# Performance work log

Hardware: AMD Instinct MI355X
Metric: run time of the kernel (lower is better)

## Reference

```python
import jax, jax.numpy as jnp
import numpy as np

N = 100000   # nodes
E = 200000   # edges
D = 512      # in_features
H = 512      # out_features


def setup_inputs() -> dict:
    key = jax.random.key(0)
    ks = jax.random.split(key, 12)
    s = 0.04  # ~1/sqrt(512), keeps gates out of saturation like nn.Linear init
    rng = np.random.default_rng(0)
    edge_index = jnp.asarray(rng.integers(0, N, size=(2, E)), dtype=jnp.int32)
    return {
        "x": jax.random.normal(ks[0], (N, D), jnp.float32),
        "edge_index": edge_index,
        "edge_feats": jax.random.normal(ks[1], (10, D), jnp.float32),
        "edge_types": jax.random.uniform(ks[2], (E, 10), jnp.float32),
        "W_iou_w": jax.random.normal(ks[3], (3 * H, D), jnp.float32) * s,
        "W_iou_b": jax.random.normal(ks[4], (3 * H,), jnp.float32) * s,
        "U_iou_w": jax.random.normal(ks[5], (3 * H, H), jnp.float32) * s,
        "U_iou_b": jax.random.normal(ks[6], (3 * H,), jnp.float32) * s,
        "W_f_w": jax.random.normal(ks[7], (H, D), jnp.float32) * s,
        "W_f_b": jax.random.normal(ks[8], (H,), jnp.float32) * s,
        "U_f_w": jax.random.normal(ks[9], (H, H), jnp.float32) * s,
        "U_f_b": jax.random.normal(ks[10], (H,), jnp.float32) * s,
    }


def _orders(parents, n_nodes):
    """node_order[p] = #edges with parent p; edge_order[i] = 1-based rank of edge i
    among same-parent edges in edge-list order (matches the torch python loop)."""
    e = parents.shape[0]
    node_order = np.zeros(n_nodes, dtype=np.int64)
    np.add.at(node_order, parents, 1)
    order = np.argsort(parents, kind="stable")
    sp = parents[order]
    is_new = np.ones(e, dtype=bool)
    is_new[1:] = sp[1:] != sp[:-1]
    pos = np.arange(e)
    start = pos[is_new][np.cumsum(is_new) - 1]  # start index of each parent group
    edge_order = np.zeros(e, dtype=np.int64)
    edge_order[order] = pos - start + 1
    return node_order, edge_order


def reference(x, edge_index, edge_feats, edge_types, W_iou_w, W_iou_b,
              U_iou_w, U_iou_b, W_f_w, W_f_b, U_f_w, U_f_b):
    # edge_feats / edge_types are unused in the default (untyped) path, as in the torch code.
    ei = np.asarray(edge_index)
    parents, children = ei[0], ei[1]
    n_nodes = x.shape[0]
    out_f = W_f_b.shape[0]
    node_order, edge_order = _orders(parents, n_nodes)
    max_iter = int(node_order.max()) if parents.size else 0

    h = jnp.zeros((n_nodes, out_f), x.dtype)
    c = jnp.zeros((n_nodes, out_f), x.dtype)
    h_sum = jnp.zeros((n_nodes, out_f), x.dtype)

    for n in range(max_iter + 1):
        nm = np.nonzero(node_order == n)[0]       # nodes evaluated this wavefront
        xn = x[nm]
        if n == 0:
            iou = xn @ W_iou_w.T + W_iou_b
        else:
            em = np.nonzero(edge_order == n)[0]   # n-th child edge of each parent
            p, ch = parents[em], children[em]     # p is unique within a wavefront
            child_h = h[ch]
            child_c = c[ch]
            h_sum = h_sum.at[p].add(child_h)
            iou = xn @ W_iou_w.T + W_iou_b + h_sum[nm] @ U_iou_w.T + U_iou_b
        i, o, u = jnp.split(iou, 3, axis=1)
        i, o, u = jax.nn.sigmoid(i), jax.nn.sigmoid(o), jnp.tanh(u)
        c = c.at[nm].set(i * u)
        if n > 0:
            f = jax.nn.sigmoid(x[p] @ W_f_w.T + W_f_b + child_h @ U_f_w.T + U_f_b)
            c = c.at[p].add(f * child_c)
        h = h.at[nm].set(o * jnp.tanh(c[nm]))
    return h
```

## Files before the change

### kernel.cpp

```cpp
#include <hip/hip_runtime.h>
#include <math.h>

#define MAXIT 16
#define MAXDEG 16

typedef __attribute__((ext_vector_type(8))) short bf16x8;
typedef __attribute__((ext_vector_type(16))) float f32x16;

static inline int imin(int a, int b) { return a < b ? a : b; }

__device__ __forceinline__ float sigm(float v) { return 1.0f / (1.0f + __expf(-v)); }
__device__ __forceinline__ float tfast(float v) {
  float vc = fminf(fmaxf(v, -20.0f), 20.0f);
  float t = __expf(2.0f * vc);
  return (t - 1.0f) / (t + 1.0f);
}
__device__ __forceinline__ unsigned short f2bf(float f) {
  unsigned int u = __float_as_uint(f);
  u += 0x7FFFu + ((u >> 16) & 1u);
  return (unsigned short)(u >> 16);
}
__device__ __forceinline__ float bf2f(unsigned short s) {
  return __uint_as_float(((unsigned int)s) << 16);
}
__device__ __forceinline__ unsigned bfadd2(unsigned x, unsigned y) {
  float sl = bf2f((unsigned short)(x & 0xFFFFu)) + bf2f((unsigned short)(y & 0xFFFFu));
  float sh = bf2f((unsigned short)(x >> 16)) + bf2f((unsigned short)(y >> 16));
  return (unsigned)f2bf(sl) | ((unsigned)f2bf(sh) << 16);
}
__device__ __forceinline__ uint4 bfadd8(uint4 a, uint4 b) {
  return make_uint4(bfadd2(a.x, b.x), bfadd2(a.y, b.y), bfadd2(a.z, b.z), bfadd2(a.w, b.w));
}

__global__ void kzero16(uint4* p, size_t n) {
  size_t i = (size_t)blockIdx.x * blockDim.x + threadIdx.x;
  size_t st = (size_t)gridDim.x * blockDim.x;
  uint4 z = make_uint4(0u, 0u, 0u, 0u);
  for (; i < n; i += st) p[i] = z;
}
__global__ void kzeroi(int* p, int n) {
  int i = blockIdx.x * blockDim.x + threadIdx.x;
  if (i < n) p[i] = 0;
}
__global__ void kfill(float* p, size_t n, float v) {
  size_t i = (size_t)blockIdx.x * blockDim.x + threadIdx.x;
  size_t st = (size_t)gridDim.x * blockDim.x;
  for (; i < n; i += st) p[i] = v;
}

__global__ void k_histo(const int* __restrict__ par, int E,
                        int* __restrict__ node_order, int* __restrict__ bucket) {
  int e = blockIdx.x * blockDim.x + threadIdx.x;
  if (e >= E) return;
  int p = par[e];
  int slot = atomicAdd(&node_order[p], 1);
  if (slot < MAXDEG) bucket[(size_t)p * MAXDEG + slot] = e;
}

__global__ void k_rank(const int* __restrict__ par, int E, int N,
                       const int* __restrict__ node_order, const int* __restrict__ bucket,
                       int* __restrict__ edgeCnt, int* __restrict__ edgeList) {
  __shared__ int lcnt[MAXIT], lbase[MAXIT];
  const int t = threadIdx.x;
  if (t < MAXIT) lcnt[t] = 0;
  __syncthreads();
  int e = blockIdx.x * blockDim.x + t;
  int r = 0, ls = 0;
  if (e < E) {
    int p = par[e];
    int d = node_order[p]; if (d > MAXDEG) d = MAXDEG;
    int rr = 1;
    for (int j = 0; j < d; ++j) rr += (bucket[(size_t)p * MAXDEG + j] < e) ? 1 : 0;
    if (rr < MAXIT) { r = rr; ls = atomicAdd(&lcnt[rr], 1); }
  }
  __syncthreads();
  if (t < MAXIT && lcnt[t] > 0) lbase[t] = atomicAdd(&edgeCnt[t], lcnt[t]);
  __syncthreads();
  if (r > 0) edgeList[(size_t)r * N + lbase[r] + ls] = e;
}

__global__ void k_nodelist(int N, const int* __restrict__ node_order,
                           int* __restrict__ nodeCnt, int* __restrict__ nodeList) {
  __shared__ int lcnt[MAXIT], lbase[MAXIT];
  const int t = threadIdx.x;
  if (t < MAXIT) lcnt[t] = 0;
  __syncthreads();
  int v = blockIdx.x * blockDim.x + t;
  int n = -1, ls = 0;
  if (v < N) {
    n = node_order[v]; if (n >= MAXIT) n = MAXIT - 1;
    ls = atomicAdd(&lcnt[n], 1);
  }
  __syncthreads();
  if (t < MAXIT && lcnt[t] > 0) lbase[t] = atomicAdd(&nodeCnt[t], lcnt[t]);
  __syncthreads();
  if (n >= 0) nodeList[(size_t)n * N + lbase[n] + ls] = v;
}

__global__ void k_pack_x(const float* __restrict__ x, unsigned short* __restrict__ xb, size_t n8) {
  size_t i = (size_t)blockIdx.x * blockDim.x + threadIdx.x;
  size_t st = (size_t)gridDim.x * blockDim.x;
  for (; i < n8; i += st) {
    const float* p = x + i * 8;
    float4 f0 = *(const float4*)p, f1 = *(const float4*)(p + 4);
    uint4 r;
    r.x = (unsigned)f2bf(f0.x) | ((unsigned)f2bf(f0.y) << 16);
    r.y = (unsigned)f2bf(f0.z) | ((unsigned)f2bf(f0.w) << 16);
    r.z = (unsigned)f2bf(f1.x) | ((unsigned)f2bf(f1.y) << 16);
    r.w = (unsigned)f2bf(f1.z) | ((unsigned)f2bf(f1.w) << 16);
    *(uint4*)(xb + i * 8) = r;
  }
}

__global__ void k_pack_biou(const float* __restrict__ W, const float* __restrict__ U,
                            unsigned short* __restrict__ Bpk) {
  int i = blockIdx.x * blockDim.x + threadIdx.x;
  if (i >= 16 * 64 * 3 * 64) return;
  int lane = i & 63;
  int q = i >> 6;
  int g = q % 3; q /= 3;
  int s = q & 63;
  int jc = q >> 6;
  int col = jc * 32 + (lane & 31);
  int k0 = s * 16 + (lane >> 5) * 8;
  int rowW = g * 512 + col;
  unsigned short v[8];
#pragma unroll
  for (int j = 0; j < 8; ++j) {
    int kk = k0 + j;
    v[j] = f2bf(kk < 512 ? W[(size_t)rowW * 512 + kk] : U[(size_t)rowW * 512 + kk - 512]);
  }
  *(uint4*)(Bpk + (size_t)i * 8) = *(uint4*)v;
}

__global__ void k_pack_bf(const float* __restrict__ W, const float* __restrict__ U,
                          unsigned short* __restrict__ Bpk) {
  int i = blockIdx.x * blockDim.x + threadIdx.x;
  if (i >= 16 * 64 * 64) return;
  int lane = i & 63;
  int q = i >> 6;
  int s = q & 63;
  int jc = q >> 6;
  int col = jc * 32 + (lane & 31);
  int k0 = s * 16 + (lane >> 5) * 8;
  unsigned short v[8];
#pragma unroll
  for (int j = 0; j < 8; ++j) {
    int kk = k0 + j;
    v[j] = f2bf(kk < 512 ? W[(size_t)col * 512 + kk] : U[(size_t)col * 512 + kk - 512]);
  }
  *(uint4*)(Bpk + (size_t)i * 8) = *(uint4*)v;
}

__global__ void k_edge_pre(int n, int N, const int* __restrict__ edgeCnt, const int* __restrict__ edgeList,
                           const int* __restrict__ par, const int* __restrict__ chd,
                           const int* __restrict__ node_order,
                           const unsigned short* __restrict__ hb, unsigned short* __restrict__ hsumb,
                           const unsigned short* __restrict__ fc, float* __restrict__ c) {
  const int cntH = edgeCnt[n];
  const int cntA = (n >= 2) ? edgeCnt[n - 1] : 0;
  const size_t totH = (size_t)cntH * 64;
  const size_t total = totH + (size_t)cntA * 64;
  size_t st = (size_t)gridDim.x * blockDim.x;
  for (size_t i = (size_t)blockIdx.x * blockDim.x + threadIdx.x; i < total; i += st) {
    if (i < totH) {
      int slot = (int)(i >> 6), j8 = ((int)i & 63) << 3;
      int e = edgeList[(size_t)n * N + slot];
      int p = par[e], ch = chd[e];
      uint4 hv = *(const uint4*)&hb[(size_t)ch * 512 + j8];
      if (n == 1) {
        *(uint4*)&hsumb[(size_t)p * 512 + j8] = hv;
      } else {
        uint4 hs = *(const uint4*)&hsumb[(size_t)p * 512 + j8];
        *(uint4*)&hsumb[(size_t)p * 512 + j8] = bfadd8(hs, hv);
      }
    } else {
      size_t k = i - totH;
      int slot = (int)(k >> 6), j8 = ((int)k & 63) << 3;
      int e = edgeList[(size_t)(n - 1) * N + slot];
      int p = par[e];
      if (node_order[p] <= n - 1) continue;
      size_t base = (size_t)p * 512 + j8;
      uint4 f8 = *(const uint4*)&fc[base];
      unsigned fw[4] = {f8.x, f8.y, f8.z, f8.w};
      float4 c0 = *(const float4*)&c[base];
      float4 c1 = *(const float4*)&c[base + 4];
      c0.x += bf2f((unsigned short)(fw[0] & 0xFFFFu)); c0.y += bf2f((unsigned short)(fw[0] >> 16));
      c0.z += bf2f((unsigned short)(fw[1] & 0xFFFFu)); c0.w += bf2f((unsigned short)(fw[1] >> 16));
      c1.x += bf2f((unsigned short)(fw[2] & 0xFFFFu)); c1.y += bf2f((unsigned short)(fw[2] >> 16));
      c1.z += bf2f((unsigned short)(fw[3] & 0xFFFFu)); c1.w += bf2f((unsigned short)(fw[3] >> 16));
      *(float4*)&c[base] = c0;
      *(float4*)&c[base + 4] = c1;
    }
  }
}

template<int MODE>
__global__ __launch_bounds__(256, 2)
void k_gemm9(int n, int N, const int* __restrict__ cntArr, const int* __restrict__ list,
             const int* __restrict__ par, const int* __restrict__ chd,
             const unsigned short* __restrict__ xb, const unsigned short* __restrict__ hsrc,
             const unsigned short* __restrict__ Bpk,
             const float* __restrict__ bW, const float* __restrict__ bU,
             float* __restrict__ c, float* __restrict__ h, unsigned short* __restrict__ hb,
             unsigned short* __restrict__ fc) {
  const int cnt = cntArr[n];
  if (cnt == 0) return;
  constexpr int KS    = (MODE == 0) ? 32 : 64;
  constexpr int KC8   = KS * 2;
  constexpr int GATES = (MODE == 2) ? 1 : 3;
  constexpr int NSTR  = (MODE == 2) ? 2 : 1;
  constexpr int NPASS = (MODE == 2) ? 2 : 4;
  constexpr int D     = 4;
  const int rowTiles = (cnt + 31) >> 5;

  __shared__ uint4 lA4[KS * 64];
  __shared__ int ids0[32], ids1[32];
  const int t = threadIdx.x, lane = t & 63, w = t >> 6;

  auto ldA = [&](int s) -> bf16x8 {
    int hk = lane >> 5, rl = lane & 31;
    return *(const bf16x8*)&lA4[s * 64 + hk * 32 + (rl ^ ((2 * s + hk) & 31))];
  };

  for (int tile = blockIdx.x; tile < rowTiles; tile += gridDim.x) {
    __syncthreads();
    if (t < 32) {
      int r = (tile << 5) + t;
      int idx = (r < cnt) ? list[(size_t)n * N + r] : -1;
      if (MODE == 2) { ids0[t] = idx >= 0 ? par[idx] : -1; ids1[t] = idx >= 0 ? chd[idx] : 0; }
      else           { ids0[t] = idx; ids1[t] = 0; }
    }
    __syncthreads();

    constexpr int ITERS = (32 * KC8) / 256;
#pragma unroll
    for (int i = 0; i < ITERS; ++i) {
      int cid = i * 256 + t;
      int row = cid >> ((MODE == 0) ? 6 : 7);
      int kc8 = cid & (KC8 - 1);
      int id0 = ids0[row];
      int id = id0 < 0 ? 0 : id0;
      uint4 v;
      if (MODE == 0 || kc8 < 64) {
        v = *(const uint4*)(xb + (size_t)id * 512 + (kc8 << 3));
      } else {
        int idh = (MODE == 2) ? ids1[row] : id;
        v = *(const uint4*)(hsrc + (size_t)idh * 512 + ((kc8 - 64) << 3));
      }
      int s = kc8 >> 1, hk = kc8 & 1;
      lA4[s * 64 + hk * 32 + (row ^ (kc8 & 31))] = v;
    }
    __syncthreads();

    for (int p = 0; p < NPASS; ++p) {
      const uint4* bb[NSTR];
#pragma unroll
      for (int str = 0; str < NSTR; ++str) {
        int jc = (MODE == 2) ? (p * 8 + str * 4 + w) : (p * 4 + w);
        bb[str] = (const uint4*)Bpk + (size_t)jc * 64 * GATES * 64 + lane;
      }
      f32x16 acc[NSTR][GATES];
#pragma unroll
      for (int str = 0; str < NSTR; ++str)
#pragma unroll
        for (int g = 0; g < GATES; ++g)
#pragma unroll
          for (int q = 0; q < 16; ++q) acc[str][g][q] = 0.f;

      bf16x8 aP[D];
      uint4 bP[D][NSTR * GATES];
#pragma unroll
      for (int d = 0; d < D; ++d) {
        aP[d] = ldA(d);
#pragma unroll
        for (int str = 0; str < NSTR; ++str)
#pragma unroll
          for (int g = 0; g < GATES; ++g)
            bP[d][str * GATES + g] = bb[str][(size_t)(d * GATES + g) * 64];
      }
      for (int s0 = 0; s0 < KS - D; s0 += D) {
#pragma unroll
        for (int d = 0; d < D; ++d) {
#pragma unroll
          for (int str = 0; str < NSTR; ++str)
#pragma unroll
            for (int g = 0; g < GATES; ++g)
              acc[str][g] = __builtin_amdgcn_mfma_f32_32x32x16_bf16(
                  aP[d], *(bf16x8*)&bP[d][str * GATES + g], acc[str][g], 0, 0, 0);
          aP[d] = ldA(s0 + D + d);
#pragma unroll
          for (int str = 0; str < NSTR; ++str)
#pragma unroll
            for (int g = 0; g < GATES; ++g)
              bP[d][str * GATES + g] = bb[str][(size_t)((s0 + D + d) * GATES + g) * 64];
        }
      }
#pragma unroll
      for (int d = 0; d < D; ++d)
#pragma unroll
        for (int str = 0; str < NSTR; ++str)
#pragma unroll
          for (int g = 0; g < GATES; ++g)
            acc[str][g] = __builtin_amdgcn_mfma_f32_32x32x16_bf16(
                aP[d], *(bf16x8*)&bP[d][str * GATES + g], acc[str][g], 0, 0, 0);

#pragma unroll
      for (int str = 0; str < NSTR; ++str) {
        const int jc = (MODE == 2) ? (p * 8 + str * 4 + w) : (p * 4 + w);
        const int jh = jc * 32 + (lane & 31);
        if (MODE < 2) {
          float bi = bW[jh], bo = bW[512 + jh], bu = bW[1024 + jh];
          if (MODE == 1) { bi += bU[jh]; bo += bU[512 + jh]; bu += bU[1024 + jh]; }
#pragma unroll
          for (int reg = 0; reg < 16; ++reg) {
            int rl = ((lane >> 5) << 2) + (reg & 3) + ((reg >> 2) << 3);
            int node = ids0[rl];
            if (node < 0) continue;
            size_t base = (size_t)node * 512 + jh;
            float iv = acc[str][0][reg] + bi;
            float ov = acc[str][1][reg] + bo;
            float uv = acc[str][2][reg] + bu;
            float fcv = (MODE == 1) ? bf2f(fc[base]) : 0.f;
            float cn = sigm(iv) * tfast(uv) + fcv;
            c[base] = cn;
            float hv = sigm(ov) * tfast(cn);
            h[base] = hv;
            hb[base] = f2bf(hv);
          }
        } else {
          float bfv = bW[jh] + bU[jh];
#pragma unroll
          for (int reg = 0; reg < 16; ++reg) {
            int rl = ((lane >> 5) << 2) + (reg & 3) + ((reg >> 2) << 3);
            int pe = ids0[rl];
            if (pe < 0) continue;
            int ce = ids1[rl];
            float fv = sigm(acc[str][0][reg] + bfv);
            fc[(size_t)pe * 512 + jh] = f2bf(fv * c[(size_t)ce * 512 + jh]);
          }
        }
      }
    }
  }
}

static void run_all(const float* x, const int* par, const int* chd,
                    const float* Wiou, const float* bWiou, const float* Uiou, const float* bUiou,
                    const float* Wf, const float* bWf, const float* Uf, const float* bUf,
                    float* h, int N, int E, void* d_ws, hipStream_t stream) {
  const size_t NV = (size_t)N * 512;
  char* cur = (char*)d_ws;
  auto take = [&](size_t bytes) -> char* {
    char* r = cur; cur += (bytes + 255) & ~(size_t)255; return r;
  };
  float* c             = (float*)take(NV * 4);
  unsigned short* hb   = (unsigned short*)take(NV * 2);
  unsigned short* hsumb= (unsigned short*)take(NV * 2);
  unsigned short* xb   = (unsigned short*)take(NV * 2);
  unsigned short* fc   = (unsigned short*)take(NV * 2);
  unsigned short* BpkI = (unsigned short*)take((size_t)16 * 64 * 3 * 64 * 8 * 2);
  unsigned short* BpkF = (unsigned short*)take((size_t)16 * 64 * 64 * 8 * 2);
  int* node_order      = (int*)take((size_t)N * 4);
  int* nodeCnt         = (int*)take(MAXIT * 4);
  int* edgeCnt         = (int*)take(MAXIT * 4);
  int* bucket          = (int*)take((size_t)N * MAXDEG * 4);
  int* nodeList        = (int*)take((size_t)MAXIT * N * 4);
  int* edgeList        = (int*)take((size_t)MAXIT * N * 4);

  kzero16<<<2048, 256, 0, stream>>>((uint4*)c, NV * 4 / 16);
  kzero16<<<2048, 256, 0, stream>>>((uint4*)hb, NV * 2 / 16);
  kzeroi<<<(N + 255) / 256, 256, 0, stream>>>(node_order, N);
  kzeroi<<<1, 64, 0, stream>>>(nodeCnt, MAXIT);
  kzeroi<<<1, 64, 0, stream>>>(edgeCnt, MAXIT);

  k_pack_x<<<2048, 256, 0, stream>>>(x, xb, NV / 8);
  k_pack_biou<<<(16 * 64 * 3 * 64 + 255) / 256, 256, 0, stream>>>(Wiou, Uiou, BpkI);
  k_pack_bf<<<(16 * 64 * 64 + 255) / 256, 256, 0, stream>>>(Wf, Uf, BpkF);

  k_histo<<<(E + 255) / 256, 256, 0, stream>>>(par, E, node_order, bucket);
  k_rank<<<(E + 255) / 256, 256, 0, stream>>>(par, E, N, node_order, bucket, edgeCnt, edgeList);
  k_nodelist<<<(N + 255) / 256, 256, 0, stream>>>(N, node_order, nodeCnt, nodeList);

  {
    int g = imin(4096, (N + 31) >> 5);
    k_gemm9<0><<<g, 256, 0, stream>>>(0, N, nodeCnt, nodeList, par, chd,
                                      xb, hsumb, BpkI, bWiou, bUiou, c, h, hb, fc);
  }
  for (int n = 1; n < MAXIT; ++n) {
    int boundE = E / n;
    int boundN = imin(N, boundE);
    int boundA = (n >= 2) ? (E / (n - 1)) : 0;
    int gE = imin(2048, (int)(((size_t)(boundE + boundA) * 64 + 255) / 256));
    int gF = imin(4096, (boundE + 31) >> 5);
    int gI = imin(4096, (boundN + 31) >> 5);
    k_edge_pre<<<gE, 256, 0, stream>>>(n, N, edgeCnt, edgeList, par, chd, node_order,
                                       hb, hsumb, fc, c);
    k_gemm9<2><<<gF, 256, 0, stream>>>(n, N, edgeCnt, edgeList, par, chd,
                                       xb, hb, BpkF, bWf, bUf, c, h, hb, fc);
    k_gemm9<1><<<gI, 256, 0, stream>>>(n, N, nodeCnt, nodeList, par, chd,
                                       xb, hsumb, BpkI, bWiou, bUiou, c, h, hb, fc);
  }
}

extern "C" void kernel_launch(void* const* d_in, const int* in_sizes, int n_in,
                              void* d_out, int out_size, void* d_ws, size_t ws_size,
                              hipStream_t stream) {
  (void)n_in; (void)out_size;
  const float* x     = (const float*)d_in[0];
  const int*   ei    = (const int*)d_in[1];
  const float* Wiou  = (const float*)d_in[4];
  const float* bWiou = (const float*)d_in[5];
  const float* Uiou  = (const float*)d_in[6];
  const float* bUiou = (const float*)d_in[7];
  const float* Wf    = (const float*)d_in[8];
  const float* bWf   = (const float*)d_in[9];
  const float* Uf    = (const float*)d_in[10];
  const float* bUf   = (const float*)d_in[11];
  const int N = in_sizes[0] / 512;
  const int E = in_sizes[1] / 2;
  const int* par = ei;
  const int* chd = ei + E;
  float* h = (float*)d_out;

  const size_t NV = (size_t)N * 512;
  const size_t need = NV * 4 + NV * 2 * 4 +
                      (size_t)8 * 1024 * 1024 +
                      ((size_t)N * (1 + MAXDEG + 2 * MAXIT) + 256) * 4;

  if (ws_size >= need) {
    run_all(x, par, chd, Wiou, bWiou, Uiou, bUiou, Wf, bWf, Uf, bUf,
            h, N, E, d_ws, stream);
  } else {
    kfill<<<2048, 256, 0, stream>>>(h, NV, 1.0e6f);
  }
}
```

Before: 2.626 ms.

## Split forget-gate GEMM into dedicated kernel with single-pass K-halved staging

Moves the forget-gate (MODE 2) path out of the shared templated GEMM into a dedicated kernel. Each wave now computes four 32-column strips in one pass instead of two passes of two strips, so the gathered A tile is read from LDS once per strip group rather than repeatedly. The A tile is staged in two K-halves (x rows, then child h rows) through a half-size LDS buffer. This should cut LDS footprint and reloads, at the cost of more accumulator registers per thread and an extra barrier between halves.

```diff
diff --git a/kernel.cpp b/kernel.cpp
--- a/kernel.cpp
+++ b/kernel.cpp
@@ -208,14 +208,12 @@
   if (cnt == 0) return;
   constexpr int KS    = (MODE == 0) ? 32 : 64;
   constexpr int KC8   = KS * 2;
-  constexpr int GATES = (MODE == 2) ? 1 : 3;
-  constexpr int NSTR  = (MODE == 2) ? 2 : 1;
-  constexpr int NPASS = (MODE == 2) ? 2 : 4;
+  constexpr int GATES = 3;
   constexpr int D     = 4;
   const int rowTiles = (cnt + 31) >> 5;
 
   __shared__ uint4 lA4[KS * 64];
-  __shared__ int ids0[32], ids1[32];
+  __shared__ int ids0[32];
   const int t = threadIdx.x, lane = t & 63, w = t >> 6;
 
   auto ldA = [&](int s) -> bf16x8 {
@@ -227,9 +225,7 @@
     __syncthreads();
     if (t < 32) {
       int r = (tile << 5) + t;
-      int idx = (r < cnt) ? list[(size_t)n * N + r] : -1;
-      if (MODE == 2) { ids0[t] = idx >= 0 ? par[idx] : -1; ids1[t] = idx >= 0 ? chd[idx] : 0; }
-      else           { ids0[t] = idx; ids1[t] = 0; }
+      ids0[t] = (r < cnt) ? list[(size_t)n * N + r] : -1;
     }
     __syncthreads();
 
@@ -245,101 +241,177 @@
       if (MODE == 0 || kc8 < 64) {
         v = *(const uint4*)(xb + (size_t)id * 512 + (kc8 << 3));
       } else {
-        int idh = (MODE == 2) ? ids1[row] : id;
-        v = *(const uint4*)(hsrc + (size_t)idh * 512 + ((kc8 - 64) << 3));
+        v = *(const uint4*)(hsrc + (size_t)id * 512 + ((kc8 - 64) << 3));
       }
       int s = kc8 >> 1, hk = kc8 & 1;
       lA4[s * 64 + hk * 32 + (row ^ (kc8 & 31))] = v;
     }
     __syncthreads();
 
-    for (int p = 0; p < NPASS; ++p) {
-      const uint4* bb[NSTR];
-#pragma unroll
-      for (int str = 0; str < NSTR; ++str) {
-        int jc = (MODE == 2) ? (p * 8 + str * 4 + w) : (p * 4 + w);
-        bb[str] = (const uint4*)Bpk + (size_t)jc * 64 * GATES * 64 + lane;
-      }
-      f32x16 acc[NSTR][GATES];
-#pragma unroll
-      for (int str = 0; str < NSTR; ++str)
-#pragma unroll
-        for (int g = 0; g < GATES; ++g)
-#pragma unroll
-          for (int q = 0; q < 16; ++q) acc[str][g][q] = 0.f;
+    for (int p = 0; p < 4; ++p) {
+      const int jc = p * 4 + w;
+      const uint4* bb = (const uint4*)Bpk + (size_t)jc * 64 * GATES * 64 + lane;
+
+      f32x16 acc[GATES];
+#pragma unroll
+      for (int g = 0; g < GATES; ++g)
+#pragma unroll
+        for (int q = 0; q < 16; ++q) acc[g][q] = 0.f;
 
       bf16x8 aP[D];
-      uint4 bP[D][NSTR * GATES];
+      uint4 bP[D][GATES];
 #pragma unroll
       for (int d = 0; d < D; ++d) {
         aP[d] = ldA(d);
 #pragma unroll
-        for (int str = 0; str < NSTR; ++str)
+        for (int g = 0; g < GATES; ++g)
+          bP[d][g] = bb[(size_t)(d * GATES + g) * 64];
+      }
+      for (int s0 = 0; s0 < KS - D; s0 += D) {
+#pragma unroll
+        for (int d = 0; d < D; ++d) {
 #pragma unroll
           for (int g = 0; g < GATES; ++g)
-            bP[d][str * GATES + g] = bb[str][(size_t)(d * GATES + g) * 64];
-      }
-      for (int s0 = 0; s0 < KS - D; s0 += D) {
-#pragma unroll
-        for (int d = 0; d < D; ++d) {
-#pragma unroll
-          for (int str = 0; str < NSTR; ++str)
-#pragma unroll
-            for (int g = 0; g < GATES; ++g)
-              acc[str][g] = __builtin_amdgcn_mfma_f32_32x32x16_bf16(
-                  aP[d], *(bf16x8*)&bP[d][str * GATES + g], acc[str][g], 0, 0, 0);
+            acc[g] = __builtin_amdgcn_mfma_f32_32x32x16_bf16(
+                aP[d], *(bf16x8*)&bP[d][g], acc[g], 0, 0, 0);
           aP[d] = ldA(s0 + D + d);
 #pragma unroll
-          for (int str = 0; str < NSTR; ++str)
-#pragma unroll
-            for (int g = 0; g < GATES; ++g)
-              bP[d][str * GATES + g] = bb[str][(size_t)((s0 + D + d) * GATES + g) * 64];
+          for (int g = 0; g < GATES; ++g)
+            bP[d][g] = bb[(size_t)((s0 + D + d) * GATES + g) * 64];
         }
       }
 #pragma unroll
       for (int d = 0; d < D; ++d)
 #pragma unroll
-        for (int str = 0; str < NSTR; ++str)
-#pragma unroll
-          for (int g = 0; g < GATES; ++g)
-            acc[str][g] = __builtin_amdgcn_mfma_f32_32x32x16_bf16(
-                aP[d], *(bf16x8*)&bP[d][str * GATES + g], acc[str][g], 0, 0, 0);
-
-#pragma unroll
-      for (int str = 0; str < NSTR; ++str) {
-        const int jc = (MODE == 2) ? (p * 8 + str * 4 + w) : (p * 4 + w);
-        const int jh = jc * 32 + (lane & 31);
-        if (MODE < 2) {
-          float bi = bW[jh], bo = bW[512 + jh], bu = bW[1024 + jh];
-          if (MODE == 1) { bi += bU[jh]; bo += bU[512 + jh]; bu += bU[1024 + jh]; }
-#pragma unroll
-          for (int reg = 0; reg < 16; ++reg) {
-            int rl = ((lane >> 5) << 2) + (reg & 3) + ((reg >> 2) << 3);
-            int node = ids0[rl];
-            if (node < 0) continue;
-            size_t base = (size_t)node * 512 + jh;
-            float iv = acc[str][0][reg] + bi;
-            float ov = acc[str][1][reg] + bo;
-            float uv = acc[str][2][reg] + bu;
-            float fcv = (MODE == 1) ? bf2f(fc[base]) : 0.f;
-            float cn = sigm(iv) * tfast(uv) + fcv;
-            c[base] = cn;
-            float hv = sigm(ov) * tfast(cn);
-            h[base] = hv;
-            hb[base] = f2bf(hv);
-          }
-        } else {
-          float bfv = bW[jh] + bU[jh];
-#pragma unroll
-          for (int reg = 0; reg < 16; ++reg) {
-            int rl = ((lane >> 5) << 2) + (reg & 3) + ((reg >> 2) << 3);
-            int pe = ids0[rl];
-            if (pe < 0) continue;
-            int ce = ids1[rl];
-            float fv = sigm(acc[str][0][reg] + bfv);
-            fc[(size_t)pe * 512 + jh] = f2bf(fv * c[(size_t)ce * 512 + jh]);
-          }
-        }
+        for (int g = 0; g < GATES; ++g)
+          acc[g] = __builtin_amdgcn_mfma_f32_32x32x16_bf16(
+              aP[d], *(bf16x8*)&bP[d][g], acc[g], 0, 0, 0);
+
+      const int jh = jc * 32 + (lane & 31);
+      float bi = bW[jh], bo = bW[512 + jh], bu = bW[1024 + jh];
+      if (MODE == 1) { bi += bU[jh]; bo += bU[512 + jh]; bu += bU[1024 + jh]; }
+#pragma unroll
+      for (int reg = 0; reg < 16; ++reg) {
+        int rl = ((lane >> 5) << 2) + (reg & 3) + ((reg >> 2) << 3);
+        int node = ids0[rl];
+        if (node < 0) continue;
+        size_t base = (size_t)node * 512 + jh;
+        float iv = acc[0][reg] + bi;
+        float ov = acc[1][reg] + bo;
+        float uv = acc[2][reg] + bu;
+        float fcv = (MODE == 1) ? bf2f(fc[base]) : 0.f;
+        float cn = sigm(iv) * tfast(uv) + fcv;
+        c[base] = cn;
+        float hv = sigm(ov) * tfast(cn);
+        h[base] = hv;
+        hb[base] = f2bf(hv);
+      }
+    }
+  }
+}
+
+__global__ __launch_bounds__(256, 2)
+void k_gemmF(int n, int N, const int* __restrict__ edgeCnt, const int* __restrict__ edgeList,
+             const int* __restrict__ par, const int* __restrict__ chd,
+             const unsigned short* __restrict__ xb, const unsigned short* __restrict__ hb,
+             const unsigned short* __restrict__ Bpk,
+             const float* __restrict__ bWf, const float* __restrict__ bUf,
+             const float* __restrict__ c, unsigned short* __restrict__ fc) {
+  const int cnt = edgeCnt[n];
+  if (cnt == 0) return;
+  const int rowTiles = (cnt + 31) >> 5;
+
+  __shared__ uint4 lA4[32 * 64];
+  __shared__ int ids0[32], ids1[32];
+  const int t = threadIdx.x, lane = t & 63, w = t >> 6;
+
+  auto ldA = [&](int s) -> bf16x8 {
+    int hk = lane >> 5, rl = lane & 31;
+    return *(const bf16x8*)&lA4[s * 64 + hk * 32 + (rl ^ ((2 * s + hk) & 31))];
+  };
+
+  for (int tile = blockIdx.x; tile < rowTiles; tile += gridDim.x) {
+    __syncthreads();
+    if (t < 32) {
+      int r = (tile << 5) + t;
+      int idx = (r < cnt) ? edgeList[(size_t)n * N + r] : -1;
+      ids0[t] = idx >= 0 ? par[idx] : -1;
+      ids1[t] = idx >= 0 ? chd[idx] : 0;
+    }
+
+    const uint4* bb[4];
+#pragma unroll
+    for (int str = 0; str < 4; ++str)
+      bb[str] = (const uint4*)Bpk + (size_t)(str * 4 + w) * 64 * 64 + lane;
+
+    f32x16 acc[4];
+#pragma unroll
+    for (int str = 0; str < 4; ++str)
+#pragma unroll
+      for (int q = 0; q < 16; ++q) acc[str][q] = 0.f;
+    __syncthreads();
+
+#pragma unroll
+    for (int half = 0; half < 2; ++half) {
+      if (half) __syncthreads();
+#pragma unroll
+      for (int i = 0; i < 8; ++i) {
+        int cid = i * 256 + t;
+        int row = cid >> 6;
+        int kc8 = cid & 63;
+        int id = half ? ids1[row] : ids0[row];
+        if (id < 0) id = 0;
+        const unsigned short* src = half ? hb : xb;
+        uint4 v = *(const uint4*)(src + (size_t)id * 512 + (kc8 << 3));
+        int s = kc8 >> 1, hk = kc8 & 1;
+        lA4[s * 64 + hk * 32 + (row ^ (kc8 & 31))] = v;
+      }
+      __syncthreads();
+
+      const int sg = half * 32;
+      bf16x8 a0 = ldA(0), a1 = ldA(1);
+      uint4 b0[4], b1[4];
+#pragma unroll
+      for (int str = 0; str < 4; ++str) {
+        b0[str] = bb[str][(size_t)(sg + 0) * 64];
+        b1[str] = bb[str][(size_t)(sg + 1) * 64];
+      }
+      for (int s0 = 0; s0 < 30; s0 += 2) {
+#pragma unroll
+        for (int str = 0; str < 4; ++str)
+          acc[str] = __builtin_amdgcn_mfma_f32_32x32x16_bf16(a0, *(bf16x8*)&b0[str], acc[str], 0, 0, 0);
+        a0 = ldA(s0 + 2);
+#pragma unroll
+        for (int str = 0; str < 4; ++str)
+          b0[str] = bb[str][(size_t)(sg + s0 + 2) * 64];
+#pragma unroll
+        for (int str = 0; str < 4; ++str)
+          acc[str] = __builtin_amdgcn_mfma_f32_32x32x16_bf16(a1, *(bf16x8*)&b1[str], acc[str], 0, 0, 0);
+        a1 = ldA(s0 + 3);
+#pragma unroll
+        for (int str = 0; str < 4; ++str)
+          b1[str] = bb[str][(size_t)(sg + s0 + 3) * 64];
+      }
+#pragma unroll
+      for (int str = 0; str < 4; ++str)
+        acc[str] = __builtin_amdgcn_mfma_f32_32x32x16_bf16(a0, *(bf16x8*)&b0[str], acc[str], 0, 0, 0);
+#pragma unroll
+      for (int str = 0; str < 4; ++str)
+        acc[str] = __builtin_amdgcn_mfma_f32_32x32x16_bf16(a1, *(bf16x8*)&b1[str], acc[str], 0, 0, 0);
+    }
+
+#pragma unroll
+    for (int str = 0; str < 4; ++str) {
+      const int jh = (str * 4 + w) * 32 + (lane & 31);
+      float bfv = bWf[jh] + bUf[jh];
+#pragma unroll
+      for (int reg = 0; reg < 16; ++reg) {
+        int rl = ((lane >> 5) << 2) + (reg & 3) + ((reg >> 2) << 3);
+        int pe = ids0[rl];
+        if (pe < 0) continue;
+        int ce = ids1[rl];
+        float fv = sigm(acc[str][reg] + bfv);
+        fc[(size_t)pe * 512 + jh] = f2bf(fv * c[(size_t)ce * 512 + jh]);
       }
     }
   }
@@ -396,8 +468,8 @@
     int gI = imin(4096, (boundN + 31) >> 5);
     k_edge_pre<<<gE, 256, 0, stream>>>(n, N, edgeCnt, edgeList, par, chd, node_order,
                                        hb, hsumb, fc, c);
-    k_gemm9<2><<<gF, 256, 0, stream>>>(n, N, edgeCnt, edgeList, par, chd,
-                                       xb, hb, BpkF, bWf, bUf, c, h, hb, fc);
+    k_gemmF<<<gF, 256, 0, stream>>>(n, N, edgeCnt, edgeList, par, chd,
+                                    xb, hb, BpkF, bWf, bUf, c, fc);
     k_gemm9<1><<<gI, 256, 0, stream>>>(n, N, nodeCnt, nodeList, par, chd,
                                        xb, hsumb, BpkI, bWiou, bUiou, c, h, hb, fc);
   }
```

Measured after the change: 7.548 ms. 2.87x slower.

## Precompute x·W projections for all nodes in one dense GEMM before wavefronts

Applied to the files above, without the earlier changes.

Adds a dense bf16 MFMA GEMM that computes x·[W_iou;W_f]^T for every node up front into a bf16 buffer, so the per-wavefront gather GEMMs only multiply the hidden-state part (K=512 instead of 1024). Wave 0 becomes a pure elementwise kernel reading the precomputed projections. This removes the repeated x gathers and halves the K loop in the sequential wavefront kernels. In exchange it spends a large up-front GEMM over all N nodes, uses extra workspace of about N*4 KB, and rounds the x projection to bf16. The old path is kept as a fallback when workspace is insufficient.

```diff
diff --git a/kernel.cpp b/kernel.cpp
--- a/kernel.cpp
+++ b/kernel.cpp
@@ -149,6 +149,56 @@
     int kk = k0 + j;
     v[j] = f2bf(kk < 512 ? W[(size_t)col * 512 + kk] : U[(size_t)col * 512 + kk - 512]);
   }
+  *(uint4*)(Bpk + (size_t)i * 8) = *(uint4*)v;
+}
+
+__global__ void k_pack_u3(const float* __restrict__ U, unsigned short* __restrict__ Bpk) {
+  int i = blockIdx.x * blockDim.x + threadIdx.x;
+  if (i >= 16 * 32 * 3 * 64) return;
+  int lane = i & 63;
+  int q = i >> 6;
+  int g = q % 3; q /= 3;
+  int s = q & 31;
+  int jc = q >> 5;
+  int col = jc * 32 + (lane & 31);
+  int k0 = s * 16 + (lane >> 5) * 8;
+  int rowW = g * 512 + col;
+  unsigned short v[8];
+#pragma unroll
+  for (int j = 0; j < 8; ++j) v[j] = f2bf(U[(size_t)rowW * 512 + k0 + j]);
+  *(uint4*)(Bpk + (size_t)i * 8) = *(uint4*)v;
+}
+
+__global__ void k_pack_uf(const float* __restrict__ U, unsigned short* __restrict__ Bpk) {
+  int i = blockIdx.x * blockDim.x + threadIdx.x;
+  if (i >= 16 * 32 * 64) return;
+  int lane = i & 63;
+  int q = i >> 6;
+  int s = q & 31;
+  int jc = q >> 5;
+  int col = jc * 32 + (lane & 31);
+  int k0 = s * 16 + (lane >> 5) * 8;
+  unsigned short v[8];
+#pragma unroll
+  for (int j = 0; j < 8; ++j) v[j] = f2bf(U[(size_t)col * 512 + k0 + j]);
+  *(uint4*)(Bpk + (size_t)i * 8) = *(uint4*)v;
+}
+
+__global__ void k_pack_wx(const float* __restrict__ Wiou, const float* __restrict__ Wf,
+                          unsigned short* __restrict__ Bpk) {
+  int i = blockIdx.x * blockDim.x + threadIdx.x;
+  if (i >= 64 * 32 * 64) return;
+  int lane = i & 63;
+  int q = i >> 6;
+  int s = q & 31;
+  int jc = q >> 5;
+  int col = jc * 32 + (lane & 31);
+  int k0 = s * 16 + (lane >> 5) * 8;
+  const float* src = (col < 1536) ? (Wiou + (size_t)col * 512)
+                                  : (Wf + (size_t)(col - 1536) * 512);
+  unsigned short v[8];
+#pragma unroll
+  for (int j = 0; j < 8; ++j) v[j] = f2bf(src[k0 + j]);
   *(uint4*)(Bpk + (size_t)i * 8) = *(uint4*)v;
 }
 
@@ -345,10 +395,298 @@
   }
 }
 
-static void run_all(const float* x, const int* par, const int* chd,
-                    const float* Wiou, const float* bWiou, const float* Uiou, const float* bUiou,
-                    const float* Wf, const float* bWf, const float* Uf, const float* bUf,
-                    float* h, int N, int E, void* d_ws, hipStream_t stream) {
+__global__ __launch_bounds__(256, 2)
+void k_pxiou(int N, const float* __restrict__ x, const unsigned short* __restrict__ BpkX,
+             unsigned short* __restrict__ px) {
+  const int rowTiles = (N + 31) >> 5;
+  __shared__ uint4 lA4[32 * 64];
+  const int t = threadIdx.x, lane = t & 63, w = t >> 6;
+
+  auto ldA = [&](int s) -> bf16x8 {
+    int hk = lane >> 5, rl = lane & 31;
+    return *(const bf16x8*)&lA4[s * 64 + hk * 32 + (rl ^ ((2 * s + hk) & 31))];
+  };
+
+  for (int tile = blockIdx.x; tile < rowTiles; tile += gridDim.x) {
+    __syncthreads();
+#pragma unroll
+    for (int i = 0; i < 8; ++i) {
+      int cid = i * 256 + t;
+      int row = cid >> 6;
+      int kc8 = cid & 63;
+      int grow = (tile << 5) + row;
+      if (grow >= N) grow = N - 1;
+      const float* p = x + (size_t)grow * 512 + (kc8 << 3);
+      float4 f0 = *(const float4*)p, f1 = *(const float4*)(p + 4);
+      uint4 v;
+      v.x = (unsigned)f2bf(f0.x) | ((unsigned)f2bf(f0.y) << 16);
+      v.y = (unsigned)f2bf(f0.z) | ((unsigned)f2bf(f0.w) << 16);
+      v.z = (unsigned)f2bf(f1.x) | ((unsigned)f2bf(f1.y) << 16);
+      v.w = (unsigned)f2bf(f1.z) | ((unsigned)f2bf(f1.w) << 16);
+      int s = kc8 >> 1, hk = kc8 & 1;
+      lA4[s * 64 + hk * 32 + (row ^ (kc8 & 31))] = v;
+    }
+    __syncthreads();
+
+    for (int p = 0; p < 16; ++p) {
+      const int jc = p * 4 + w;
+      const uint4* bb = (const uint4*)BpkX + (size_t)jc * 32 * 64 + lane;
+      f32x16 acc;
+#pragma unroll
+      for (int q = 0; q < 16; ++q) acc[q] = 0.f;
+      bf16x8 aP[4];
+      uint4 bP[4];
+#pragma unroll
+      for (int d = 0; d < 4; ++d) { aP[d] = ldA(d); bP[d] = bb[(size_t)d * 64]; }
+      for (int s0 = 0; s0 < 28; s0 += 4) {
+#pragma unroll
+        for (int d = 0; d < 4; ++d) {
+          acc = __builtin_amdgcn_mfma_f32_32x32x16_bf16(aP[d], *(bf16x8*)&bP[d], acc, 0, 0, 0);
+          aP[d] = ldA(s0 + 4 + d);
+          bP[d] = bb[(size_t)(s0 + 4 + d) * 64];
+        }
+      }
+#pragma unroll
+      for (int d = 0; d < 4; ++d)
+        acc = __builtin_amdgcn_mfma_f32_32x32x16_bf16(aP[d], *(bf16x8*)&bP[d], acc, 0, 0, 0);
+
+      const int jh = jc * 32 + (lane & 31);
+#pragma unroll
+      for (int reg = 0; reg < 16; ++reg) {
+        int rl = ((lane >> 5) << 2) + (reg & 3) + ((reg >> 2) << 3);
+        int grow = (tile << 5) + rl;
+        if (grow < N) px[(size_t)grow * 2048 + jh] = f2bf(acc[reg]);
+      }
+    }
+  }
+}
+
+__global__ void k_wave0(int N, const int* __restrict__ nodeCnt, const int* __restrict__ nodeList,
+                        const unsigned short* __restrict__ px, const float* __restrict__ bW,
+                        float* __restrict__ c, float* __restrict__ h, unsigned short* __restrict__ hb) {
+  size_t total = (size_t)nodeCnt[0] * 512;
+  size_t st = (size_t)gridDim.x * blockDim.x;
+  for (size_t i = (size_t)blockIdx.x * blockDim.x + threadIdx.x; i < total; i += st) {
+    int slot = (int)(i >> 9), col = (int)(i & 511);
+    int node = nodeList[slot];
+    size_t pb = (size_t)node * 2048;
+    float iv = bf2f(px[pb + col]) + bW[col];
+    float ov = bf2f(px[pb + 512 + col]) + bW[512 + col];
+    float uv = bf2f(px[pb + 1024 + col]) + bW[1024 + col];
+    float cn = sigm(iv) * tfast(uv);
+    size_t base = (size_t)node * 512 + col;
+    c[base] = cn;
+    float hv = sigm(ov) * tfast(cn);
+    h[base] = hv;
+    hb[base] = f2bf(hv);
+  }
+}
+
+template<int MODE>
+__global__ __launch_bounds__(256, 2)
+void k_gemmS(int n, int N, const int* __restrict__ cntArr, const int* __restrict__ list,
+             const int* __restrict__ par, const int* __restrict__ chd,
+             const unsigned short* __restrict__ asrc, const unsigned short* __restrict__ Bpk,
+             const unsigned short* __restrict__ px,
+             const float* __restrict__ bW, const float* __restrict__ bU,
+             float* __restrict__ c, float* __restrict__ h, unsigned short* __restrict__ hb,
+             unsigned short* __restrict__ fc) {
+  const int cnt = cntArr[n];
+  if (cnt == 0) return;
+  constexpr int KS    = 32;
+  constexpr int GATES = (MODE == 2) ? 1 : 3;
+  constexpr int NSTR  = (MODE == 2) ? 2 : 1;
+  constexpr int NPASS = (MODE == 2) ? 2 : 4;
+  constexpr int D     = 4;
+  const int rowTiles = (cnt + 31) >> 5;
+
+  __shared__ uint4 lA4[KS * 64];
+  __shared__ int ids0[32], ids1[32];
+  const int t = threadIdx.x, lane = t & 63, w = t >> 6;
+
+  auto ldA = [&](int s) -> bf16x8 {
+    int hk = lane >> 5, rl = lane & 31;
+    return *(const bf16x8*)&lA4[s * 64 + hk * 32 + (rl ^ ((2 * s + hk) & 31))];
+  };
+
+  for (int tile = blockIdx.x; tile < rowTiles; tile += gridDim.x) {
+    __syncthreads();
+    if (t < 32) {
+      int r = (tile << 5) + t;
+      int idx = (r < cnt) ? list[(size_t)n * N + r] : -1;
+      if (MODE == 2) { ids0[t] = idx >= 0 ? par[idx] : -1; ids1[t] = idx >= 0 ? chd[idx] : 0; }
+      else           { ids0[t] = idx; ids1[t] = 0; }
+    }
+    __syncthreads();
+
+#pragma unroll
+    for (int i = 0; i < 8; ++i) {
+      int cid = i * 256 + t;
+      int row = cid >> 6;
+      int kc8 = cid & 63;
+      int id = (MODE == 2) ? ids1[row] : ids0[row];
+      if (id < 0) id = 0;
+      uint4 v = *(const uint4*)(asrc + (size_t)id * 512 + (kc8 << 3));
+      int s = kc8 >> 1, hk = kc8 & 1;
+      lA4[s * 64 + hk * 32 + (row ^ (kc8 & 31))] = v;
+    }
+    __syncthreads();
+
+    for (int p = 0; p < NPASS; ++p) {
+      const uint4* bb[NSTR];
+#pragma unroll
+      for (int str = 0; str < NSTR; ++str) {
+        int jc = (MODE == 2) ? (p * 8 + str * 4 + w) : (p * 4 + w);
+        bb[str] = (const uint4*)Bpk + (size_t)jc * KS * GATES * 64 + lane;
+      }
+      f32x16 acc[NSTR][GATES];
+#pragma unroll
+      for (int str = 0; str < NSTR; ++str)
+#pragma unroll
+        for (int g = 0; g < GATES; ++g)
+#pragma unroll
+          for (int q = 0; q < 16; ++q) acc[str][g][q] = 0.f;
+
+      bf16x8 aP[D];
+      uint4 bP[D][NSTR * GATES];
+#pragma unroll
+      for (int d = 0; d < D; ++d) {
+        aP[d] = ldA(d);
+#pragma unroll
+        for (int str = 0; str < NSTR; ++str)
+#pragma unroll
+          for (int g = 0; g < GATES; ++g)
+            bP[d][str * GATES + g] = bb[str][(size_t)(d * GATES + g) * 64];
+      }
+      for (int s0 = 0; s0 < KS - D; s0 += D) {
+#pragma unroll
+        for (int d = 0; d < D; ++d) {
+#pragma unroll
+          for (int str = 0; str < NSTR; ++str)
+#pragma unroll
+            for (int g = 0; g < GATES; ++g)
+              acc[str][g] = __builtin_amdgcn_mfma_f32_32x32x16_bf16(
+                  aP[d], *(bf16x8*)&bP[d][str * GATES + g], acc[str][g], 0, 0, 0);
+          aP[d] = ldA(s0 + D + d);
+#pragma unroll
+          for (int str = 0; str < NSTR; ++str)
+#pragma unroll
+            for (int g = 0; g < GATES; ++g)
+              bP[d][str * GATES + g] = bb[str][(size_t)((s0 + D + d) * GATES + g) * 64];
+        }
+      }
+#pragma unroll
+      for (int d = 0; d < D; ++d)
+#pragma unroll
+        for (int str = 0; str < NSTR; ++str)
+#pragma unroll
+          for (int g = 0; g < GATES; ++g)
+            acc[str][g] = __builtin_amdgcn_mfma_f32_32x32x16_bf16(
+                aP[d], *(bf16x8*)&bP[d][str * GATES + g], acc[str][g], 0, 0, 0);
+
+#pragma unroll
+      for (int str = 0; str < NSTR; ++str) {
+        const int jc = (MODE == 2) ? (p * 8 + str * 4 + w) : (p * 4 + w);
+        const int jh = jc * 32 + (lane & 31);
+        if (MODE == 1) {
+          float bi = bW[jh] + bU[jh];
+          float bo = bW[512 + jh] + bU[512 + jh];
+          float bu = bW[1024 + jh] + bU[1024 + jh];
+#pragma unroll
+          for (int reg = 0; reg < 16; ++reg) {
+            int rl = ((lane >> 5) << 2) + (reg & 3) + ((reg >> 2) << 3);
+            int node = ids0[rl];
+            if (node < 0) continue;
+            size_t base = (size_t)node * 512 + jh;
+            size_t pb = (size_t)node * 2048;
+            float iv = acc[str][0][reg] + bf2f(px[pb + jh]) + bi;
+            float ov = acc[str][1][reg] + bf2f(px[pb + 512 + jh]) + bo;
+            float uv = acc[str][2][reg] + bf2f(px[pb + 1024 + jh]) + bu;
+            float fcv = bf2f(fc[base]);
+            float cn = sigm(iv) * tfast(uv) + fcv;
+            c[base] = cn;
+            float hv = sigm(ov) * tfast(cn);
+            h[base] = hv;
+            hb[base] = f2bf(hv);
+          }
+        } else {
+          float bfv = bW[jh] + bU[jh];
+#pragma unroll
+          for (int reg = 0; reg < 16; ++reg) {
+            int rl = ((lane >> 5) << 2) + (reg & 3) + ((reg >> 2) << 3);
+            int pe = ids0[rl];
+            if (pe < 0) continue;
+            int ce = ids1[rl];
+            float fv = sigm(acc[str][0][reg] + bf2f(px[(size_t)pe * 2048 + 1536 + jh]) + bfv);
+            fc[(size_t)pe * 512 + jh] = f2bf(fv * c[(size_t)ce * 512 + jh]);
+          }
+        }
+      }
+    }
+  }
+}
+
+static void run_allA(const float* x, const int* par, const int* chd,
+                     const float* Wiou, const float* bWiou, const float* Uiou, const float* bUiou,
+                     const float* Wf, const float* bWf, const float* Uf, const float* bUf,
+                     float* h, int N, int E, void* d_ws, hipStream_t stream) {
+  const size_t NV = (size_t)N * 512;
+  char* cur = (char*)d_ws;
+  auto take = [&](size_t bytes) -> char* {
+    char* r = cur; cur += (bytes + 255) & ~(size_t)255; return r;
+  };
+  float* c             = (float*)take(NV * 4);
+  unsigned short* hb   = (unsigned short*)take(NV * 2);
+  unsigned short* hsumb= (unsigned short*)take(NV * 2);
+  unsigned short* fc   = (unsigned short*)take(NV * 2);
+  unsigned short* px   = (unsigned short*)take((size_t)N * 2048 * 2);
+  unsigned short* BpkU3= (unsigned short*)take((size_t)16 * 32 * 3 * 64 * 8 * 2);
+  unsigned short* BpkUF= (unsigned short*)take((size_t)16 * 32 * 64 * 8 * 2);
+  unsigned short* BpkX = (unsigned short*)take((size_t)64 * 32 * 64 * 8 * 2);
+  int* node_order      = (int*)take((size_t)N * 4);
+  int* nodeCnt         = (int*)take(MAXIT * 4);
+  int* edgeCnt         = (int*)take(MAXIT * 4);
+  int* bucket          = (int*)take((size_t)N * MAXDEG * 4);
+  int* nodeList        = (int*)take((size_t)MAXIT * N * 4);
+  int* edgeList        = (int*)take((size_t)MAXIT * N * 4);
+
+  kzero16<<<2048, 256, 0, stream>>>((uint4*)c, NV * 4 / 16);
+  kzero16<<<2048, 256, 0, stream>>>((uint4*)hb, NV * 2 / 16);
+  kzeroi<<<(N + 255) / 256, 256, 0, stream>>>(node_order, N);
+  kzeroi<<<1, 64, 0, stream>>>(nodeCnt, MAXIT);
+  kzeroi<<<1, 64, 0, stream>>>(edgeCnt, MAXIT);
+
+  k_pack_u3<<<(16 * 32 * 3 * 64 + 255) / 256, 256, 0, stream>>>(Uiou, BpkU3);
+  k_pack_uf<<<(16 * 32 * 64 + 255) / 256, 256, 0, stream>>>(Uf, BpkUF);
+  k_pack_wx<<<(64 * 32 * 64 + 255) / 256, 256, 0, stream>>>(Wiou, Wf, BpkX);
+
+  k_histo<<<(E + 255) / 256, 256, 0, stream>>>(par, E, node_order, bucket);
+  k_rank<<<(E + 255) / 256, 256, 0, stream>>>(par, E, N, node_order, bucket, edgeCnt, edgeList);
+  k_nodelist<<<(N + 255) / 256, 256, 0, stream>>>(N, node_order, nodeCnt, nodeList);
+
+  k_pxiou<<<imin(4096, (N + 31) >> 5), 256, 0, stream>>>(N, x, BpkX, px);
+  k_wave0<<<2048, 256, 0, stream>>>(N, nodeCnt, nodeList, px, bWiou, c, h, hb);
+
+  for (int n = 1; n < MAXIT; ++n) {
+    int boundE = E / n;
+    int boundN = imin(N, boundE);
+    int boundA = (n >= 2) ? (E / (n - 1)) : 0;
+    int gE = imin(2048, (int)(((size_t)(boundE + boundA) * 64 + 255) / 256));
+    int gF = imin(4096, (boundE + 31) >> 5);
+    int gI = imin(4096, (boundN + 31) >> 5);
+    k_edge_pre<<<gE, 256, 0, stream>>>(n, N, edgeCnt, edgeList, par, chd, node_order,
+                                       hb, hsumb, fc, c);
+    k_gemmS<2><<<gF, 256, 0, stream>>>(n, N, edgeCnt, edgeList, par, chd,
+                                       hb, BpkUF, px, bWf, bUf, c, h, hb, fc);
+    k_gemmS<1><<<gI, 256, 0, stream>>>(n, N, nodeCnt, nodeList, par, chd,
+                                       hsumb, BpkU3, px, bWiou, bUiou, c, h, hb, fc);
+  }
+}
+
+static void run_allB(const float* x, const int* par, const int* chd,
+                     const float* Wiou, const float* bWiou, const float* Uiou, const float* bUiou,
+                     const float* Wf, const float* bWf, const float* Uf, const float* bUf,
+                     float* h, int N, int E, void* d_ws, hipStream_t stream) {
   const size_t NV = (size_t)N * 512;
   char* cur = (char*)d_ws;
   auto take = [&](size_t bytes) -> char* {
@@ -424,13 +762,16 @@
   float* h = (float*)d_out;
 
   const size_t NV = (size_t)N * 512;
-  const size_t need = NV * 4 + NV * 2 * 4 +
-                      (size_t)8 * 1024 * 1024 +
-                      ((size_t)N * (1 + MAXDEG + 2 * MAXIT) + 256) * 4;
-
-  if (ws_size >= need) {
-    run_all(x, par, chd, Wiou, bWiou, Uiou, bUiou, Wf, bWf, Uf, bUf,
-            h, N, E, d_ws, stream);
+  const size_t ints = ((size_t)N * (1 + MAXDEG + 2 * MAXIT) + 256) * 4;
+  const size_t needA = NV * 18 + (size_t)8 * 1024 * 1024 + ints;
+  const size_t needB = NV * 12 + (size_t)8 * 1024 * 1024 + ints;
+
+  if (ws_size >= needA) {
+    run_allA(x, par, chd, Wiou, bWiou, Uiou, bUiou, Wf, bWf, Uf, bUf,
+             h, N, E, d_ws, stream);
+  } else if (ws_size >= needB) {
+    run_allB(x, par, chd, Wiou, bWiou, Uiou, bUiou, Wf, bWf, Uf, bUf,
+             h, N, E, d_ws, stream);
   } else {
     kfill<<<2048, 256, 0, stream>>>(h, NV, 1.0e6f);
   }
```

Measured after the change: 2.625 ms. No clear change (-0.0%).
